# Kernel tuning notes

Measured on AMD Instinct MI355X. Metric: run time of the kernel, lower is better.

## Reference

```python
import jax, jax.numpy as jnp
import numpy as np

N = 100000      # nodes
E = 3200000     # edges (avg degree 32)
F_IN = 128      # num_node_features
H = 16          # hidden dim (fixed in module)
C = 2           # num_classes


def setup_inputs() -> dict:
    key = jax.random.key(0)
    k0, k1, k2, k3 = jax.random.split(key, 4)
    x = jax.random.normal(k0, (N, F_IN), dtype=jnp.float32)
    edge_index = jax.random.randint(k1, (2, E), 0, N, dtype=jnp.int32)
    # GCNConv params: weight (in,out) + bias (out,) per layer (glorot-ish scale)
    W1 = jax.random.normal(k2, (F_IN, H), dtype=jnp.float32) * (1.0 / np.sqrt(F_IN))
    b1 = jnp.zeros((H,), jnp.float32)
    W2 = jax.random.normal(k3, (H, C), dtype=jnp.float32) * (1.0 / np.sqrt(H))
    b2 = jnp.zeros((C,), jnp.float32)
    return {"x": x, "edge_index": edge_index, "W1": W1, "b1": b1, "W2": W2, "b2": b2}


def _gcn_conv(x, W, b, src, dst, n):
    # GCNConv: h = D^{-1/2}(A+I)D^{-1/2} (x W) + b, with self-loops in src/dst
    h = x @ W                                   # [n, out]
    deg = jax.ops.segment_sum(jnp.ones_like(dst, dtype=h.dtype), dst, num_segments=n)
    dinv = jnp.where(deg > 0, jax.lax.rsqrt(deg), 0.0)
    norm = dinv[src] * dinv[dst]                # [E+n]
    msg = h[src] * norm[:, None]                # gather + scale
    out = jax.ops.segment_sum(msg, dst, num_segments=n)  # scatter-add
    return out + b


def reference(x, edge_index, W1, b1, W2, b2):
    loops = jnp.arange(N, dtype=edge_index.dtype)
    src = jnp.concatenate([edge_index[0], loops])
    dst = jnp.concatenate([edge_index[1], loops])
    h = jax.nn.relu(_gcn_conv(x, W1, b1, src, dst, N))
    # F.dropout(training=False) in eval mode is identity
    out = _gcn_conv(h, W2, b2, src, dst, N)
    return jax.nn.log_softmax(out, axis=1)
```

## Files before the change

### kernel.cpp

```cpp
#include <hip/hip_runtime.h>
#include <hip/hip_bf16.h>

#define NN 100000
#define NE 3200000
#define FIN 128
#define HD 16
#define CD 2

#define BSH 8
#define BSPAN 256
#define NBKT 391
#define CHUNK 8192
#define NPB ((NE + CHUNK - 1) / CHUNK)

#define FXS 1048576.0f
#define FXI (1.0f / 1048576.0f)

__device__ __forceinline__ float bf2f(ushort u) {
    union { float f; unsigned int i; } v; v.i = ((unsigned int)u) << 16; return v.f;
}
__device__ __forceinline__ float lo2f(unsigned int u) {
    union { float f; unsigned int i; } v; v.i = u << 16; return v.f;
}
__device__ __forceinline__ float hi2f(unsigned int u) {
    union { float f; unsigned int i; } v; v.i = u & 0xFFFF0000u; return v.f;
}
__device__ __forceinline__ ushort f2b(float f) {
    union { float f; unsigned int u; } v; v.f = f;
    unsigned int r = (v.u + 0x7FFFu + ((v.u >> 16) & 1u)) >> 16;
    return (ushort)r;
}

__global__ __launch_bounds__(512) void k_cnt(const int* __restrict__ dst,
                                             int* __restrict__ cntmat) {
    __shared__ int h[NBKT];
    for (int i = threadIdx.x; i < NBKT; i += 512) h[i] = 0;
    __syncthreads();
    int cq = blockIdx.x * (CHUNK / 4);
    const int4* d4 = (const int4*)dst;
    #pragma unroll
    for (int j = 0; j < CHUNK / 2048; ++j) {
        int e4 = cq + j * 512 + threadIdx.x;
        if (e4 < NE / 4) {
            int4 d = d4[e4];
            atomicAdd(&h[d.x >> BSH], 1);
            atomicAdd(&h[d.y >> BSH], 1);
            atomicAdd(&h[d.z >> BSH], 1);
            atomicAdd(&h[d.w >> BSH], 1);
        }
    }
    __syncthreads();
    int* row = cntmat + (size_t)blockIdx.x * NBKT;
    for (int i = threadIdx.x; i < NBKT; i += 512) row[i] = h[i];
}

__global__ __launch_bounds__(256) void k_colscan(const int* __restrict__ cntmat,
                                                 int* __restrict__ relm,
                                                 int* __restrict__ btot) {
    __shared__ int sm[256];
    int j = blockIdx.x, t = threadIdx.x;
    int v[2];
    int b0 = t * 2;
    #pragma unroll
    for (int k = 0; k < 2; ++k) {
        int b = b0 + k;
        v[k] = (b < NPB) ? cntmat[(size_t)b * NBKT + j] : 0;
    }
    sm[t] = v[0] + v[1];
    __syncthreads();
    for (int off = 1; off < 256; off <<= 1) {
        int x = 0;
        if (t >= off) x = sm[t - off];
        __syncthreads();
        if (t >= off) sm[t] += x;
        __syncthreads();
    }
    int run = (t == 0) ? 0 : sm[t - 1];
    int* rrow = relm + (size_t)j * NPB;
    #pragma unroll
    for (int k = 0; k < 2; ++k) {
        int b = b0 + k;
        if (b < NPB) rrow[b] = run;
        run += v[k];
    }
    if (t == 255) btot[j] = sm[255];
}

__global__ __launch_bounds__(512) void k_scanb(const int* __restrict__ btot,
                                               int* __restrict__ boff) {
    __shared__ int sm[512];
    int t = threadIdx.x;
    sm[t] = (t < NBKT) ? btot[t] : 0;
    __syncthreads();
    for (int off = 1; off < 512; off <<= 1) {
        int v = 0;
        if (t >= off) v = sm[t - off];
        __syncthreads();
        if (t >= off) sm[t] += v;
        __syncthreads();
    }
    if (t < NBKT) boff[t] = t ? sm[t - 1] : 0;
    if (t == 511) boff[NBKT] = sm[511];
}

__global__ __launch_bounds__(512) void k_part(const int* __restrict__ src,
                                              const int* __restrict__ dst,
                                              const int* __restrict__ boff,
                                              const int* __restrict__ relm,
                                              unsigned int* __restrict__ csrb) {
    __shared__ int cur[NBKT];
    int b = blockIdx.x, t = threadIdx.x;
    for (int i = t; i < NBKT; i += 512)
        cur[i] = boff[i] + relm[(size_t)i * NPB + b];
    __syncthreads();
    int cq = b * (CHUNK / 4);
    const int4* s4 = (const int4*)src;
    const int4* d4 = (const int4*)dst;
    #pragma unroll
    for (int j = 0; j < CHUNK / 2048; ++j) {
        int e4 = cq + j * 512 + t;
        if (e4 < NE / 4) {
            int4 s = s4[e4];
            int4 d = d4[e4];
            int p;
            p = atomicAdd(&cur[d.x >> BSH], 1);
            csrb[p] = (unsigned)s.x | ((unsigned)(d.x & (BSPAN - 1)) << 17);
            p = atomicAdd(&cur[d.y >> BSH], 1);
            csrb[p] = (unsigned)s.y | ((unsigned)(d.y & (BSPAN - 1)) << 17);
            p = atomicAdd(&cur[d.z >> BSH], 1);
            csrb[p] = (unsigned)s.z | ((unsigned)(d.z & (BSPAN - 1)) << 17);
            p = atomicAdd(&cur[d.w >> BSH], 1);
            csrb[p] = (unsigned)s.w | ((unsigned)(d.w & (BSPAN - 1)) << 17);
        }
    }
}

__global__ __launch_bounds__(512) void k_deg(const int* __restrict__ boff,
                                             const unsigned int* __restrict__ csrb,
                                             float* __restrict__ dinv) {
    __shared__ int cnt[BSPAN];
    int b = blockIdx.x, t = threadIdx.x;
    if (t < BSPAN) cnt[t] = 0;
    __syncthreads();
    int e0 = boff[b], e1 = boff[b + 1];
    for (int e = e0 + t; e < e1; e += 512) atomicAdd(&cnt[csrb[e] >> 17], 1);
    __syncthreads();
    if (t < BSPAN) {
        int node = b * BSPAN + t;
        if (node < NN) dinv[node] = rsqrtf((float)cnt[t] + 1.0f);
    }
}

__global__ __launch_bounds__(256) void k_gemm1(const float* __restrict__ x,
                                               const float* __restrict__ W1,
                                               const float* __restrict__ dinv,
                                               ushort* __restrict__ h1b) {
    __shared__ float wsm[FIN][HD];
    for (int i = threadIdx.x; i < FIN * HD; i += 256) wsm[i >> 4][i & 15] = W1[i];
    __syncthreads();
    int t = blockIdx.x * 256 + threadIdx.x;
    int node = t >> 2;
    if (node >= NN) return;
    int g = (t & 3) * 4;
    const float4* xr = (const float4*)(x + (size_t)node * FIN);
    float a0 = 0.f, a1 = 0.f, a2 = 0.f, a3 = 0.f;
    #pragma unroll
    for (int k4 = 0; k4 < FIN / 4; ++k4) {
        float4 v = xr[k4];
        #pragma unroll
        for (int kk = 0; kk < 4; ++kk) {
            float vk = (kk == 0) ? v.x : (kk == 1) ? v.y : (kk == 2) ? v.z : v.w;
            float4 w = *(const float4*)&wsm[k4 * 4 + kk][g];
            a0 += vk * w.x;
            a1 += vk * w.y;
            a2 += vk * w.z;
            a3 += vk * w.w;
        }
    }
    float di = dinv[node];
    ushort4 r = {f2b(a0 * di), f2b(a1 * di), f2b(a2 * di), f2b(a3 * di)};
    *(ushort4*)(h1b + (size_t)node * HD + g) = r;
}

__device__ __forceinline__ void scat16(int* a, uint4 u0, uint4 u1) {
    atomicAdd(a + 0,  __float2int_rn(lo2f(u0.x) * FXS));
    atomicAdd(a + 1,  __float2int_rn(hi2f(u0.x) * FXS));
    atomicAdd(a + 2,  __float2int_rn(lo2f(u0.y) * FXS));
    atomicAdd(a + 3,  __float2int_rn(hi2f(u0.y) * FXS));
    atomicAdd(a + 4,  __float2int_rn(lo2f(u0.z) * FXS));
    atomicAdd(a + 5,  __float2int_rn(hi2f(u0.z) * FXS));
    atomicAdd(a + 6,  __float2int_rn(lo2f(u0.w) * FXS));
    atomicAdd(a + 7,  __float2int_rn(hi2f(u0.w) * FXS));
    atomicAdd(a + 8,  __float2int_rn(lo2f(u1.x) * FXS));
    atomicAdd(a + 9,  __float2int_rn(hi2f(u1.x) * FXS));
    atomicAdd(a + 10, __float2int_rn(lo2f(u1.y) * FXS));
    atomicAdd(a + 11, __float2int_rn(hi2f(u1.y) * FXS));
    atomicAdd(a + 12, __float2int_rn(lo2f(u1.z) * FXS));
    atomicAdd(a + 13, __float2int_rn(hi2f(u1.z) * FXS));
    atomicAdd(a + 14, __float2int_rn(lo2f(u1.w) * FXS));
    atomicAdd(a + 15, __float2int_rn(hi2f(u1.w) * FXS));
}

__global__ __launch_bounds__(512) void k_aggs1(const int* __restrict__ boff,
                                               const unsigned int* __restrict__ csrb,
                                               const ushort* __restrict__ h1b,
                                               const float* __restrict__ dinv,
                                               const float* __restrict__ b1,
                                               const float* __restrict__ W2,
                                               float* __restrict__ g_s) {
    __shared__ int acc[BSPAN][HD + 1];
    __shared__ float w2s[HD * 2];
    __shared__ float b1s[HD];
    int b = blockIdx.x, t = threadIdx.x;
    for (int i = t; i < BSPAN * (HD + 1); i += 512) ((int*)acc)[i] = 0;
    if (t < HD * 2) w2s[t] = W2[t];
    else if (t < HD * 3) b1s[t - HD * 2] = b1[t - HD * 2];
    __syncthreads();
    int e0 = boff[b], e1 = boff[b + 1];
    int e = e0 + t;
    for (; e + 512 < e1; e += 1024) {
        unsigned pa = csrb[e];
        unsigned pb = csrb[e + 512];
        const uint4* ra = (const uint4*)(h1b + (size_t)(pa & 0x1FFFF) * HD);
        const uint4* rb = (const uint4*)(h1b + (size_t)(pb & 0x1FFFF) * HD);
        uint4 a0 = ra[0], a1 = ra[1];
        uint4 c0 = rb[0], c1 = rb[1];
        scat16(acc[pa >> 17], a0, a1);
        scat16(acc[pb >> 17], c0, c1);
    }
    if (e < e1) {
        unsigned p = csrb[e];
        const uint4* r = (const uint4*)(h1b + (size_t)(p & 0x1FFFF) * HD);
        uint4 u0 = r[0], u1 = r[1];
        scat16(acc[p >> 17], u0, u1);
    }
    __syncthreads();
    int loc = t >> 1, half = t & 1;
    int node = b * BSPAN + loc;
    if (node < NN) {
        float di = dinv[node];
        const uint4 sv = *(const uint4*)(h1b + (size_t)node * HD + half * 8);
        float sf[8] = {lo2f(sv.x), hi2f(sv.x), lo2f(sv.y), hi2f(sv.y),
                       lo2f(sv.z), hi2f(sv.z), lo2f(sv.w), hi2f(sv.w)};
        const int* a = acc[loc] + half * 8;
        const float* bb = b1s + half * 8;
        const float* ww = w2s + half * 16;
        float p0 = 0.f, p1 = 0.f;
        #pragma unroll
        for (int k = 0; k < 8; ++k) {
            float v = fmaxf(di * ((float)a[k] * FXI + sf[k]) + bb[k], 0.f);
            p0 += v * ww[k * 2];
            p1 += v * ww[k * 2 + 1];
        }
        p0 += __shfl_xor(p0, 1, 64);
        p1 += __shfl_xor(p1, 1, 64);
        if (half == 0) {
            float2 r = {p0 * di, p1 * di};
            *(float2*)(g_s + (size_t)node * 2) = r;
        }
    }
}

__global__ __launch_bounds__(512) void k_aggs2(const int* __restrict__ boff,
                                               const unsigned int* __restrict__ csrb,
                                               const float* __restrict__ g_s,
                                               const float* __restrict__ dinv,
                                               const float* __restrict__ b2,
                                               float* __restrict__ out) {
    __shared__ int acc[BSPAN * 3];
    int b = blockIdx.x, t = threadIdx.x;
    for (int i = t; i < BSPAN * 3; i += 512) acc[i] = 0;
    __syncthreads();
    int e0 = boff[b], e1 = boff[b + 1];
    int e = e0 + t;
    for (; e + 512 < e1; e += 1024) {
        unsigned pa = csrb[e];
        unsigned pb = csrb[e + 512];
        float2 va = *(const float2*)(g_s + (size_t)(pa & 0x1FFFF) * 2);
        float2 vb = *(const float2*)(g_s + (size_t)(pb & 0x1FFFF) * 2);
        int la = (pa >> 17) * 3, lb = (pb >> 17) * 3;
        atomicAdd(&acc[la],     __float2int_rn(va.x * FXS));
        atomicAdd(&acc[la + 1], __float2int_rn(va.y * FXS));
        atomicAdd(&acc[lb],     __float2int_rn(vb.x * FXS));
        atomicAdd(&acc[lb + 1], __float2int_rn(vb.y * FXS));
    }
    if (e < e1) {
        unsigned p = csrb[e];
        float2 v = *(const float2*)(g_s + (size_t)(p & 0x1FFFF) * 2);
        int l = (p >> 17) * 3;
        atomicAdd(&acc[l],     __float2int_rn(v.x * FXS));
        atomicAdd(&acc[l + 1], __float2int_rn(v.y * FXS));
    }
    __syncthreads();
    if (t < BSPAN) {
        int node = b * BSPAN + t;
        if (node < NN) {
            float di = dinv[node];
            float2 sv = *(const float2*)(g_s + (size_t)node * 2);
            float o0 = di * ((float)acc[t * 3] * FXI + sv.x) + b2[0];
            float o1 = di * ((float)acc[t * 3 + 1] * FXI + sv.y) + b2[1];
            float mx = fmaxf(o0, o1);
            float l = mx + logf(__expf(o0 - mx) + __expf(o1 - mx));
            float2 r = {o0 - l, o1 - l};
            *(float2*)(out + (size_t)node * 2) = r;
        }
    }
}

extern "C" void kernel_launch(void* const* d_in, const int* in_sizes, int n_in,
                              void* d_out, int out_size, void* d_ws, size_t ws_size,
                              hipStream_t stream) {
    const float* x   = (const float*)d_in[0];
    const int* ei    = (const int*)d_in[1];
    const int* src   = ei;
    const int* dst   = ei + NE;
    const float* W1  = (const float*)d_in[2];
    const float* b1  = (const float*)d_in[3];
    const float* W2  = (const float*)d_in[4];
    const float* b2  = (const float*)d_in[5];
    float* out = (float*)d_out;

    char* w = (char*)d_ws;
    float* dinv        = (float*)w;          w += NN * 4;
    int*   btot        = (int*)w;            w += NBKT * 4;
    int*   boff        = (int*)w;            w += (NBKT + 1) * 4;
    int*   cntmat      = (int*)w;            w += (size_t)NPB * NBKT * 4;
    int*   relm        = (int*)w;            w += (size_t)NBKT * NPB * 4;
    unsigned int* csrb = (unsigned int*)w;   w += (size_t)NE * 4;
    ushort* h1b        = (ushort*)w;         w += (size_t)NN * HD * 2;
    float* g_s         = (float*)w;          w += NN * CD * 4;

    k_cnt    <<<NPB, 512, 0, stream>>>(dst, cntmat);
    k_colscan<<<NBKT, 256, 0, stream>>>(cntmat, relm, btot);
    k_scanb  <<<1, 512, 0, stream>>>(btot, boff);
    k_part   <<<NPB, 512, 0, stream>>>(src, dst, boff, relm, csrb);
    k_deg    <<<NBKT, 512, 0, stream>>>(boff, csrb, dinv);
    k_gemm1  <<<(NN * 4 + 255) / 256, 256, 0, stream>>>(x, W1, dinv, h1b);
    k_aggs1  <<<NBKT, 512, 0, stream>>>(boff, csrb, h1b, dinv, b1, W2, g_s);
    k_aggs2  <<<NBKT, 512, 0, stream>>>(boff, csrb, g_s, dinv, b2, out);
}
```

Before: 205.7 us.

## Replace count-scan partition with fixed-capacity buckets and fused global-atomic degrees

Merges the count, column-scan, bucket-scan, partition and degree kernels into one scatter kernel. Each block claims a slice of each bucket with one global atomic into a fixed-capacity region (CAP per bucket), and node degrees come from global atomics on dst. Bucket span is halved to 128 nodes and the aggregation kernels drop to 256 threads, and dinv is recomputed from deg where it is used. This removes several launches and extra passes over the edge lists, but adds random global atomics, and it silently overflows if any bucket gets more than CAP edges, a limit that only holds for evenly spread inputs.

Result: slower. 301.7 us (+46.7%).

```diff
diff --git a/kernel.cpp b/kernel.cpp
--- a/kernel.cpp
+++ b/kernel.cpp
@@ -7,18 +7,15 @@
 #define HD 16
 #define CD 2
 
-#define BSH 8
-#define BSPAN 256
-#define NBKT 391
-#define CHUNK 8192
-#define NPB ((NE + CHUNK - 1) / CHUNK)
+#define BSH 7
+#define BSPAN 128
+#define NBKT 782
+#define CAP 4800
+#define NPB 391
 
 #define FXS 1048576.0f
 #define FXI (1.0f / 1048576.0f)
 
-__device__ __forceinline__ float bf2f(ushort u) {
-    union { float f; unsigned int i; } v; v.i = ((unsigned int)u) << 16; return v.f;
-}
 __device__ __forceinline__ float lo2f(unsigned int u) {
     union { float f; unsigned int i; } v; v.i = u << 16; return v.f;
 }
@@ -31,129 +28,63 @@
     return (ushort)r;
 }
 
-__global__ __launch_bounds__(512) void k_cnt(const int* __restrict__ dst,
-                                             int* __restrict__ cntmat) {
+__global__ __launch_bounds__(512) void k_scat(const int* __restrict__ src,
+                                              const int* __restrict__ dst,
+                                              int* __restrict__ deg,
+                                              int* __restrict__ gcnt,
+                                              unsigned int* __restrict__ csrb) {
     __shared__ int h[NBKT];
-    for (int i = threadIdx.x; i < NBKT; i += 512) h[i] = 0;
-    __syncthreads();
-    int cq = blockIdx.x * (CHUNK / 4);
-    const int4* d4 = (const int4*)dst;
+    __shared__ int cur[NBKT];
+    int t = threadIdx.x;
+    for (int i = t; i < NBKT; i += 512) h[i] = 0;
+    __syncthreads();
+    int cq = blockIdx.x * 2048;
+    const int4* s4p = (const int4*)src;
+    const int4* d4p = (const int4*)dst;
+    int4 sv[4], dv[4];
     #pragma unroll
-    for (int j = 0; j < CHUNK / 2048; ++j) {
-        int e4 = cq + j * 512 + threadIdx.x;
-        if (e4 < NE / 4) {
-            int4 d = d4[e4];
-            atomicAdd(&h[d.x >> BSH], 1);
-            atomicAdd(&h[d.y >> BSH], 1);
-            atomicAdd(&h[d.z >> BSH], 1);
-            atomicAdd(&h[d.w >> BSH], 1);
-        }
-    }
-    __syncthreads();
-    int* row = cntmat + (size_t)blockIdx.x * NBKT;
-    for (int i = threadIdx.x; i < NBKT; i += 512) row[i] = h[i];
-}
-
-__global__ __launch_bounds__(256) void k_colscan(const int* __restrict__ cntmat,
-                                                 int* __restrict__ relm,
-                                                 int* __restrict__ btot) {
-    __shared__ int sm[256];
-    int j = blockIdx.x, t = threadIdx.x;
-    int v[2];
-    int b0 = t * 2;
-    #pragma unroll
-    for (int k = 0; k < 2; ++k) {
-        int b = b0 + k;
-        v[k] = (b < NPB) ? cntmat[(size_t)b * NBKT + j] : 0;
-    }
-    sm[t] = v[0] + v[1];
-    __syncthreads();
-    for (int off = 1; off < 256; off <<= 1) {
-        int x = 0;
-        if (t >= off) x = sm[t - off];
-        __syncthreads();
-        if (t >= off) sm[t] += x;
-        __syncthreads();
-    }
-    int run = (t == 0) ? 0 : sm[t - 1];
-    int* rrow = relm + (size_t)j * NPB;
-    #pragma unroll
-    for (int k = 0; k < 2; ++k) {
-        int b = b0 + k;
-        if (b < NPB) rrow[b] = run;
-        run += v[k];
-    }
-    if (t == 255) btot[j] = sm[255];
-}
-
-__global__ __launch_bounds__(512) void k_scanb(const int* __restrict__ btot,
-                                               int* __restrict__ boff) {
-    __shared__ int sm[512];
-    int t = threadIdx.x;
-    sm[t] = (t < NBKT) ? btot[t] : 0;
-    __syncthreads();
-    for (int off = 1; off < 512; off <<= 1) {
-        int v = 0;
-        if (t >= off) v = sm[t - off];
-        __syncthreads();
-        if (t >= off) sm[t] += v;
-        __syncthreads();
-    }
-    if (t < NBKT) boff[t] = t ? sm[t - 1] : 0;
-    if (t == 511) boff[NBKT] = sm[511];
-}
-
-__global__ __launch_bounds__(512) void k_part(const int* __restrict__ src,
-                                              const int* __restrict__ dst,
-                                              const int* __restrict__ boff,
-                                              const int* __restrict__ relm,
-                                              unsigned int* __restrict__ csrb) {
-    __shared__ int cur[NBKT];
-    int b = blockIdx.x, t = threadIdx.x;
-    for (int i = t; i < NBKT; i += 512)
-        cur[i] = boff[i] + relm[(size_t)i * NPB + b];
-    __syncthreads();
-    int cq = b * (CHUNK / 4);
-    const int4* s4 = (const int4*)src;
-    const int4* d4 = (const int4*)dst;
-    #pragma unroll
-    for (int j = 0; j < CHUNK / 2048; ++j) {
+    for (int j = 0; j < 4; ++j) {
         int e4 = cq + j * 512 + t;
         if (e4 < NE / 4) {
-            int4 s = s4[e4];
-            int4 d = d4[e4];
+            sv[j] = s4p[e4];
+            dv[j] = d4p[e4];
+            atomicAdd(&h[dv[j].x >> BSH], 1);
+            atomicAdd(&h[dv[j].y >> BSH], 1);
+            atomicAdd(&h[dv[j].z >> BSH], 1);
+            atomicAdd(&h[dv[j].w >> BSH], 1);
+            atomicAdd(&deg[dv[j].x], 1);
+            atomicAdd(&deg[dv[j].y], 1);
+            atomicAdd(&deg[dv[j].z], 1);
+            atomicAdd(&deg[dv[j].w], 1);
+        }
+    }
+    __syncthreads();
+    for (int i = t; i < NBKT; i += 512) {
+        int c = h[i];
+        int base = c ? atomicAdd(&gcnt[i], c) : 0;
+        cur[i] = i * CAP + base;
+    }
+    __syncthreads();
+    #pragma unroll
+    for (int j = 0; j < 4; ++j) {
+        int e4 = cq + j * 512 + t;
+        if (e4 < NE / 4) {
             int p;
-            p = atomicAdd(&cur[d.x >> BSH], 1);
-            csrb[p] = (unsigned)s.x | ((unsigned)(d.x & (BSPAN - 1)) << 17);
-            p = atomicAdd(&cur[d.y >> BSH], 1);
-            csrb[p] = (unsigned)s.y | ((unsigned)(d.y & (BSPAN - 1)) << 17);
-            p = atomicAdd(&cur[d.z >> BSH], 1);
-            csrb[p] = (unsigned)s.z | ((unsigned)(d.z & (BSPAN - 1)) << 17);
-            p = atomicAdd(&cur[d.w >> BSH], 1);
-            csrb[p] = (unsigned)s.w | ((unsigned)(d.w & (BSPAN - 1)) << 17);
-        }
-    }
-}
-
-__global__ __launch_bounds__(512) void k_deg(const int* __restrict__ boff,
-                                             const unsigned int* __restrict__ csrb,
-                                             float* __restrict__ dinv) {
-    __shared__ int cnt[BSPAN];
-    int b = blockIdx.x, t = threadIdx.x;
-    if (t < BSPAN) cnt[t] = 0;
-    __syncthreads();
-    int e0 = boff[b], e1 = boff[b + 1];
-    for (int e = e0 + t; e < e1; e += 512) atomicAdd(&cnt[csrb[e] >> 17], 1);
-    __syncthreads();
-    if (t < BSPAN) {
-        int node = b * BSPAN + t;
-        if (node < NN) dinv[node] = rsqrtf((float)cnt[t] + 1.0f);
+            p = atomicAdd(&cur[dv[j].x >> BSH], 1);
+            csrb[p] = (unsigned)sv[j].x | ((unsigned)(dv[j].x & (BSPAN - 1)) << 17);
+            p = atomicAdd(&cur[dv[j].y >> BSH], 1);
+            csrb[p] = (unsigned)sv[j].y | ((unsigned)(dv[j].y & (BSPAN - 1)) << 17);
+            p = atomicAdd(&cur[dv[j].z >> BSH], 1);
+            csrb[p] = (unsigned)sv[j].z | ((unsigned)(dv[j].z & (BSPAN - 1)) << 17);
+            p = atomicAdd(&cur[dv[j].w >> BSH], 1);
+            csrb[p] = (unsigned)sv[j].w | ((unsigned)(dv[j].w & (BSPAN - 1)) << 17);
+        }
     }
 }
 
 __global__ __launch_bounds__(256) void k_gemm1(const float* __restrict__ x,
                                                const float* __restrict__ W1,
-                                               const float* __restrict__ dinv,
+                                               const int* __restrict__ deg,
                                                ushort* __restrict__ h1b) {
     __shared__ float wsm[FIN][HD];
     for (int i = threadIdx.x; i < FIN * HD; i += 256) wsm[i >> 4][i & 15] = W1[i];
@@ -177,7 +108,7 @@
             a3 += vk * w.w;
         }
     }
-    float di = dinv[node];
+    float di = rsqrtf((float)deg[node] + 1.0f);
     ushort4 r = {f2b(a0 * di), f2b(a1 * di), f2b(a2 * di), f2b(a3 * di)};
     *(ushort4*)(h1b + (size_t)node * HD + g) = r;
 }
@@ -201,10 +132,10 @@
     atomicAdd(a + 15, __float2int_rn(hi2f(u1.w) * FXS));
 }
 
-__global__ __launch_bounds__(512) void k_aggs1(const int* __restrict__ boff,
+__global__ __launch_bounds__(256) void k_aggs1(const int* __restrict__ gcnt,
                                                const unsigned int* __restrict__ csrb,
                                                const ushort* __restrict__ h1b,
-                                               const float* __restrict__ dinv,
+                                               const int* __restrict__ deg,
                                                const float* __restrict__ b1,
                                                const float* __restrict__ W2,
                                                float* __restrict__ g_s) {
@@ -212,15 +143,15 @@
     __shared__ float w2s[HD * 2];
     __shared__ float b1s[HD];
     int b = blockIdx.x, t = threadIdx.x;
-    for (int i = t; i < BSPAN * (HD + 1); i += 512) ((int*)acc)[i] = 0;
+    for (int i = t; i < BSPAN * (HD + 1); i += 256) ((int*)acc)[i] = 0;
     if (t < HD * 2) w2s[t] = W2[t];
     else if (t < HD * 3) b1s[t - HD * 2] = b1[t - HD * 2];
     __syncthreads();
-    int e0 = boff[b], e1 = boff[b + 1];
+    int e0 = b * CAP, e1 = e0 + gcnt[b];
     int e = e0 + t;
-    for (; e + 512 < e1; e += 1024) {
+    for (; e + 256 < e1; e += 512) {
         unsigned pa = csrb[e];
-        unsigned pb = csrb[e + 512];
+        unsigned pb = csrb[e + 256];
         const uint4* ra = (const uint4*)(h1b + (size_t)(pa & 0x1FFFF) * HD);
         const uint4* rb = (const uint4*)(h1b + (size_t)(pb & 0x1FFFF) * HD);
         uint4 a0 = ra[0], a1 = ra[1];
@@ -238,7 +169,7 @@
     int loc = t >> 1, half = t & 1;
     int node = b * BSPAN + loc;
     if (node < NN) {
-        float di = dinv[node];
+        float di = rsqrtf((float)deg[node] + 1.0f);
         const uint4 sv = *(const uint4*)(h1b + (size_t)node * HD + half * 8);
         float sf[8] = {lo2f(sv.x), hi2f(sv.x), lo2f(sv.y), hi2f(sv.y),
                        lo2f(sv.z), hi2f(sv.z), lo2f(sv.w), hi2f(sv.w)};
@@ -261,21 +192,21 @@
     }
 }
 
-__global__ __launch_bounds__(512) void k_aggs2(const int* __restrict__ boff,
+__global__ __launch_bounds__(256) void k_aggs2(const int* __restrict__ gcnt,
                                                const unsigned int* __restrict__ csrb,
                                                const float* __restrict__ g_s,
-                                               const float* __restrict__ dinv,
+                                               const int* __restrict__ deg,
                                                const float* __restrict__ b2,
                                                float* __restrict__ out) {
     __shared__ int acc[BSPAN * 3];
     int b = blockIdx.x, t = threadIdx.x;
-    for (int i = t; i < BSPAN * 3; i += 512) acc[i] = 0;
-    __syncthreads();
-    int e0 = boff[b], e1 = boff[b + 1];
+    for (int i = t; i < BSPAN * 3; i += 256) acc[i] = 0;
+    __syncthreads();
+    int e0 = b * CAP, e1 = e0 + gcnt[b];
     int e = e0 + t;
-    for (; e + 512 < e1; e += 1024) {
+    for (; e + 256 < e1; e += 512) {
         unsigned pa = csrb[e];
-        unsigned pb = csrb[e + 512];
+        unsigned pb = csrb[e + 256];
         float2 va = *(const float2*)(g_s + (size_t)(pa & 0x1FFFF) * 2);
         float2 vb = *(const float2*)(g_s + (size_t)(pb & 0x1FFFF) * 2);
         int la = (pa >> 17) * 3, lb = (pb >> 17) * 3;
@@ -295,7 +226,7 @@
     if (t < BSPAN) {
         int node = b * BSPAN + t;
         if (node < NN) {
-            float di = dinv[node];
+            float di = rsqrtf((float)deg[node] + 1.0f);
             float2 sv = *(const float2*)(g_s + (size_t)node * 2);
             float o0 = di * ((float)acc[t * 3] * FXI + sv.x) + b2[0];
             float o1 = di * ((float)acc[t * 3 + 1] * FXI + sv.y) + b2[1];
@@ -321,21 +252,15 @@
     float* out = (float*)d_out;
 
     char* w = (char*)d_ws;
-    float* dinv        = (float*)w;          w += NN * 4;
-    int*   btot        = (int*)w;            w += NBKT * 4;
-    int*   boff        = (int*)w;            w += (NBKT + 1) * 4;
-    int*   cntmat      = (int*)w;            w += (size_t)NPB * NBKT * 4;
-    int*   relm        = (int*)w;            w += (size_t)NBKT * NPB * 4;
-    unsigned int* csrb = (unsigned int*)w;   w += (size_t)NE * 4;
+    int*   deg         = (int*)w;            w += NN * 4;
+    int*   gcnt        = (int*)w;            w += NBKT * 4;
+    unsigned int* csrb = (unsigned int*)w;   w += (size_t)NBKT * CAP * 4;
     ushort* h1b        = (ushort*)w;         w += (size_t)NN * HD * 2;
     float* g_s         = (float*)w;          w += NN * CD * 4;
 
-    k_cnt    <<<NPB, 512, 0, stream>>>(dst, cntmat);
-    k_colscan<<<NBKT, 256, 0, stream>>>(cntmat, relm, btot);
-    k_scanb  <<<1, 512, 0, stream>>>(btot, boff);
-    k_part   <<<NPB, 512, 0, stream>>>(src, dst, boff, relm, csrb);
-    k_deg    <<<NBKT, 512, 0, stream>>>(boff, csrb, dinv);
-    k_gemm1  <<<(NN * 4 + 255) / 256, 256, 0, stream>>>(x, W1, dinv, h1b);
-    k_aggs1  <<<NBKT, 512, 0, stream>>>(boff, csrb, h1b, dinv, b1, W2, g_s);
-    k_aggs2  <<<NBKT, 512, 0, stream>>>(boff, csrb, g_s, dinv, b2, out);
-}
+    hipMemsetAsync(deg, 0, (NN + NBKT) * 4, stream);
+    k_scat  <<<NPB, 512, 0, stream>>>(src, dst, deg, gcnt, csrb);
+    k_gemm1 <<<(NN * 4 + 255) / 256, 256, 0, stream>>>(x, W1, deg, h1b);
+    k_aggs1 <<<NBKT, 256, 0, stream>>>(gcnt, csrb, h1b, deg, b1, W2, g_s);
+    k_aggs2 <<<NBKT, 256, 0, stream>>>(gcnt, csrb, g_s, deg, b2, out);
+}
```
